# Kernel tuning notes

Hardware: AMD Instinct MI355X
Metric: run time of the kernel (lower is better)

Reference implementation:

```python
import jax, jax.numpy as jnp
import numpy as np

B, T, D_K, N_HEADS, D_FF, VOCAB, N_LAYERS = 4, 1024, 1024, 16, 4096, 65, 6


def setup_inputs() -> dict:
    key = jax.random.key(0)
    ks = jax.random.split(key, 12)
    f = lambda k, sh: jax.random.normal(k, sh, dtype=jnp.float32) * 0.02
    return {
        "batchData": jax.random.randint(ks[0], (B, T), 0, VOCAB),
        "target": jax.random.randint(ks[1], (B, T), 0, VOCAB),
        "pos": jnp.arange(T),
        "Wtok": f(ks[2], (VOCAB, D_K)),
        "Wpos": f(ks[3], (T, D_K)),
        "Wq": f(ks[4], (D_K, D_K)), "bq": jnp.zeros((D_K,), jnp.float32),
        "Wk": f(ks[5], (D_K, D_K)), "bk": jnp.zeros((D_K,), jnp.float32),
        "Wv": f(ks[6], (D_K, D_K)), "bv": jnp.zeros((D_K,), jnp.float32),
        "W1": f(ks[7], (D_K, D_FF)), "b1": jnp.zeros((D_FF,), jnp.float32),
        "W2": f(ks[8], (D_FF, D_K)), "b2": jnp.zeros((D_K,), jnp.float32),
        "ln_w": jnp.ones((D_K,), jnp.float32),
        "Wf": f(ks[9], (D_K, VOCAB)), "bf": jnp.zeros((VOCAB,), jnp.float32),
        "n_layers": N_LAYERS,
        "n_heads": N_HEADS,
    }


def layer_norm(x, w, eps=1e-5):
    m = jnp.mean(x, axis=-1, keepdims=True)
    v = jnp.var(x, axis=-1, keepdims=True)
    return (x - m) / jnp.sqrt(v + eps) * w


def reference(batchData, target, pos, Wtok, Wpos, Wq, bq, Wk, bk, Wv, bv,
              W1, b1, W2, b2, ln_w, Wf, bf, n_layers, n_heads):
    x = Wtok[batchData] + Wpos[pos]  # [B, T, C] (pos embedding broadcasts)
    Bsz, Tlen, C = x.shape
    dh = C // n_heads
    mask = jnp.tril(jnp.ones((Tlen, Tlen), dtype=bool))
    inv_sqrt_dk = 1.0 / jnp.sqrt(jnp.float32(C))  # source divides by sqrt(full d_k)

    def block(x):
        q = (x @ Wq + bq).reshape(Bsz, Tlen, n_heads, dh).transpose(0, 2, 1, 3)
        k = (x @ Wk + bk).reshape(Bsz, Tlen, n_heads, dh).transpose(0, 2, 1, 3)
        v = (x @ Wv + bv).reshape(Bsz, Tlen, n_heads, dh).transpose(0, 2, 1, 3)
        scores = jnp.einsum('bhqd,bhkd->bhqk', q, k) * inv_sqrt_dk
        scores = jnp.where(mask, scores, -jnp.inf)
        attn = jax.nn.softmax(scores, axis=-1)
        h = jnp.einsum('bhqk,bhkd->bhqd', attn, v)
        h = h.transpose(0, 2, 1, 3).reshape(Bsz, Tlen, C)
        h = h + layer_norm(h, ln_w)           # x = x + ln(x) (shared ln)
        ff = jax.nn.relu(h @ W1 + b1) @ W2 + b2
        return ff + layer_norm(ff, ln_w)      # same shared ln again

    # ModuleList repeats the SAME block object, so weights are shared across layers
    for _ in range(n_layers):
        x = block(x)

    logits = x @ Wf + bf                       # [B, T, V]
    probs = jax.nn.softmax(logits, axis=1)     # softmax over T, as in source
    pred = probs.reshape(Bsz * Tlen, -1)
    onehot = jax.nn.one_hot(target.reshape(-1), VOCAB, dtype=jnp.float32)
    # F.cross_entropy with soft (one-hot float) targets
    loss = -jnp.mean(jnp.sum(onehot * jax.nn.log_softmax(pred, axis=-1), axis=-1))
    return loss, probs
```

## Files before the change

### kernel.cpp

```cpp
#include <hip/hip_runtime.h>

typedef __attribute__((ext_vector_type(8))) short bh8;
typedef __attribute__((ext_vector_type(4))) float f4v;

constexpr int VOC = 65;
constexpr int NL  = 6;
constexpr int Mrow = 4096;

__device__ inline float b2f(unsigned short u) {
  union { unsigned int i; float f; } x; x.i = ((unsigned int)u) << 16; return x.f;
}
__device__ inline unsigned short f2b(float f) {
  union { float f; unsigned int i; } x; x.f = f;
  return (unsigned short)((x.i + 0x7FFFu + ((x.i >> 16) & 1u)) >> 16);
}
__device__ inline void gld16(const void* g, void* l) {
  __builtin_amdgcn_global_load_lds(
      (const __attribute__((address_space(1))) unsigned int*)g,
      (__attribute__((address_space(3))) unsigned int*)l, 16, 0, 0);
}
__device__ inline bh8 lds_swz(const unsigned short* base, int row, int colbyte) {
  int off = row * 128 + (colbyte ^ ((row & 7) << 4));
  return *(const bh8*)((const char*)base + off);
}
__device__ inline f4v mfma16(bh8 a, bh8 b, f4v c) {
  return __builtin_amdgcn_mfma_f32_16x16x32_bf16(a, b, c, 0, 0, 0);
}
#define WAITV(n) asm volatile("s_waitcnt vmcnt(" #n ")" ::: "memory")
#define WAITVL(n) asm volatile("s_waitcnt vmcnt(" #n ") lgkmcnt(0)" ::: "memory")

__global__ __launch_bounds__(256) void wt_conv(const float* __restrict__ src,
    unsigned short* __restrict__ dst, int K, int N) {
  __shared__ float t[32][33];
  int k0 = blockIdx.x * 32, n0 = blockIdx.y * 32;
  int tid = threadIdx.x;
#pragma unroll
  for (int i = 0; i < 4; ++i) {
    int idx = tid + i * 256;
    int kr = idx >> 5, nc = idx & 31;
    t[kr][nc] = (n0 + nc < N) ? src[(size_t)(k0 + kr) * N + n0 + nc] : 0.f;
  }
  __syncthreads();
#pragma unroll
  for (int i = 0; i < 4; ++i) {
    int idx = tid + i * 256;
    int nr = idx >> 5, kc = idx & 31;
    dst[(size_t)(n0 + nr) * K + k0 + kc] = f2b(t[kc][nr]);
  }
}

__global__ __launch_bounds__(256) void bias_prep(
    const float* __restrict__ bq, const float* __restrict__ bk,
    const float* __restrict__ bv, const float* __restrict__ bf,
    float* __restrict__ bqkv, float* __restrict__ bfp) {
  int i = blockIdx.x * 256 + threadIdx.x;
  if (i < 1024) bqkv[i] = bq[i];
  else if (i < 2048) bqkv[i] = bk[i - 1024];
  else if (i < 3072) bqkv[i] = bv[i - 2048];
  else if (i < 3200) bfp[i - 3072] = (i - 3072 < VOC) ? bf[i - 3072] : 0.f;
}

__global__ __launch_bounds__(256) void embed_bf(const int* __restrict__ tok,
    const float* __restrict__ Wtok, const float* __restrict__ Wpos,
    unsigned short* __restrict__ Xb) {
  int bt = blockIdx.x, t = bt & 1023, tid = threadIdx.x;
  int id = tok[bt];
  float4 a = ((const float4*)(Wtok + (size_t)id * 1024))[tid];
  float4 p = ((const float4*)(Wpos + (size_t)t * 1024))[tid];
  ushort4 o;
  o.x = f2b(a.x + p.x); o.y = f2b(a.y + p.y);
  o.z = f2b(a.z + p.z); o.w = f2b(a.w + p.w);
  ((ushort4*)(Xb + (size_t)bt * 1024))[tid] = o;
}

template <bool RELU, bool PART, bool VT>
__global__ __launch_bounds__(512) void gemm8(
    const unsigned short* __restrict__ A, const unsigned short* __restrict__ Bt,
    const float* __restrict__ bias, void* __restrict__ Cout,
    unsigned short* __restrict__ Vtout, long N, long Kloop, long lda, long ldb,
    int MT, int NT) {
  __shared__ unsigned short As[3 * 256 * 32];
  __shared__ unsigned short Bs[3 * 128 * 32];
  const int tid = threadIdx.x;
  const int lane = tid & 63, w = tid >> 6;
  const int wr = w >> 1, wc = w & 1;
  const int lr = lane & 15, lh = lane >> 4, lh4 = lh * 4;

  const int nwg = (int)gridDim.x;
  const int wid = ((int)blockIdx.x & 7) * (nwg >> 3) + ((int)blockIdx.x >> 3);
  const int rowT = wid % MT, rest = wid / MT;
  const int colT = rest % NT, ksl = rest / NT;
  const long row0 = (long)rowT * 256, col0 = (long)colT * 128;
  const long kOff = (long)ksl * Kloop;

  f4v acc[4][4];
#pragma unroll
  for (int i = 0; i < 4; ++i)
#pragma unroll
    for (int j = 0; j < 4; ++j) acc[i][j] = f4v{0.f, 0.f, 0.f, 0.f};

  const int rg = tid >> 2, s = tid & 3;
  const int ch = s ^ ((rg ^ (rg >> 2)) & 3);
  const unsigned short* ApA0 = A + (row0 + rg) * lda + kOff + ch * 8;
  const unsigned short* ApA1 = ApA0 + 128 * lda;
  const unsigned short* BpB  = Bt + (col0 + rg) * ldb + kOff + ch * 8;

  auto stage = [&](int t, int buf) {
    const long k0 = (long)t << 5;
    gld16(ApA0 + k0, &As[buf * 8192 + tid * 8]);
    gld16(ApA1 + k0, &As[buf * 8192 + 4096 + tid * 8]);
    gld16(BpB  + k0, &Bs[buf * 4096 + tid * 8]);
  };

  const int nt = (int)(Kloop >> 5);
  stage(0, 0);
  stage(1, 1);

  const int fl = (lr ^ (lr >> 2)) & 3;
  const int slot = lh ^ fl;

  for (int t = 0; t < nt; ++t) {
    if (t + 1 < nt) { WAITVL(3); } else { WAITVL(0); }
    __builtin_amdgcn_s_barrier();
    __builtin_amdgcn_sched_barrier(0);
    const unsigned short* Ab = &As[(t % 3) * 8192];
    const unsigned short* Bb = &Bs[(t % 3) * 4096];
    bh8 a[4], b[4];
#pragma unroll
    for (int mi = 0; mi < 4; ++mi)
      a[mi] = *(const bh8*)&Ab[(wr * 64 + mi * 16 + lr) * 32 + slot * 8];
#pragma unroll
    for (int ni = 0; ni < 4; ++ni)
      b[ni] = *(const bh8*)&Bb[(wc * 64 + ni * 16 + lr) * 32 + slot * 8];
    if (t + 2 < nt) stage(t + 2, (t + 2) % 3);
    __builtin_amdgcn_s_setprio(1);
#pragma unroll
    for (int mi = 0; mi < 4; ++mi)
#pragma unroll
      for (int ni = 0; ni < 4; ++ni)
        acc[mi][ni] = mfma16(a[mi], b[ni], acc[mi][ni]);
    __builtin_amdgcn_s_setprio(0);
  }

  if (PART) {
    unsigned short* P = (unsigned short*)Cout + (size_t)ksl * 4096 * 1024;
#pragma unroll
    for (int mi = 0; mi < 4; ++mi)
#pragma unroll
      for (int ni = 0; ni < 4; ++ni) {
        long col = col0 + wc * 64 + ni * 16 + lr;
#pragma unroll
        for (int r = 0; r < 4; ++r) {
          long row = row0 + wr * 64 + mi * 16 + lh4 + r;
          P[row * N + col] = f2b(acc[mi][ni][r]);
        }
      }
    return;
  }
  if (VT && col0 >= 2048) {
#pragma unroll
    for (int mi = 0; mi < 4; ++mi) {
#pragma unroll
      for (int ni = 0; ni < 4; ++ni) {
        int col = (int)col0 + wc * 64 + ni * 16 + lr;
        float bb = bias[col];
        int cc = col - 2048;
        long row = row0 + wr * 64 + mi * 16 + lh4;
        int bi = (int)(row >> 10), tt = (int)(row & 1023);
        ushort4 o;
        o.x = f2b(acc[mi][ni][0] + bb);
        o.y = f2b(acc[mi][ni][1] + bb);
        o.z = f2b(acc[mi][ni][2] + bb);
        o.w = f2b(acc[mi][ni][3] + bb);
        *(ushort4*)&Vtout[((size_t)(bi * 16 + (cc >> 6)) * 64 + (cc & 63)) *
                              1024 + tt] = o;
      }
    }
    return;
  }
#pragma unroll
  for (int mi = 0; mi < 4; ++mi) {
#pragma unroll
    for (int ni = 0; ni < 4; ++ni) {
      long col = col0 + wc * 64 + ni * 16 + lr;
      float bb = bias[col];
#pragma unroll
      for (int r = 0; r < 4; ++r) {
        long row = row0 + wr * 64 + mi * 16 + lh4 + r;
        float v = acc[mi][ni][r] + bb;
        if (RELU) v = fmaxf(v, 0.f);
        ((unsigned short*)Cout)[row * N + col] = f2b(v);
      }
    }
  }
}

template <int TM, int TN, bool RELU, bool F32OUT>
__global__ __launch_bounds__(256) void gemm4(
    const unsigned short* __restrict__ A, const unsigned short* __restrict__ Bt,
    const float* __restrict__ bias, void* __restrict__ Cout, long N, long K) {
  constexpr int MI = TM / 32, NI = TN / 32;
  constexpr int ABUF = TM * 64, BBUF = TN * 64;
  __shared__ unsigned short As[2 * ABUF];
  __shared__ unsigned short Bs[2 * BBUF];
  const int tid = threadIdx.x;
  const int lane = tid & 63, w = tid >> 6;
  const int wr = w >> 1, wc = w & 1;
  const int lr = lane & 15, lh = lane >> 4, lh4 = lh * 4;
  const long row0 = (long)blockIdx.x * TM, col0 = (long)blockIdx.y * TN;
  f4v acc[MI][NI];
#pragma unroll
  for (int i = 0; i < MI; ++i)
#pragma unroll
    for (int j = 0; j < NI; ++j) acc[i][j] = f4v{0.f, 0.f, 0.f, 0.f};
  const int rg = tid >> 3, s = tid & 7;
  const int ch = s ^ (rg & 7);
  const unsigned short* Ap = A + (row0 + rg) * K + ch * 8;
  const unsigned short* Bp = Bt + (col0 + rg) * K + ch * 8;
  auto stage = [&](int t, int buf) {
    const long k0 = (long)t << 6;
#pragma unroll
    for (int i = 0; i < MI; ++i)
      gld16(Ap + i * 32 * K + k0, &As[buf * ABUF + (i * 256 + tid) * 8]);
#pragma unroll
    for (int i = 0; i < NI; ++i)
      gld16(Bp + i * 32 * K + k0, &Bs[buf * BBUF + (i * 256 + tid) * 8]);
  };
  const int nt = (int)(K >> 6);
  stage(0, 0);
  for (int t = 0; t < nt; ++t) {
    const int cur = t & 1;
    if (t + 1 < nt) {
      stage(t + 1, cur ^ 1);
      WAITV(6);
    } else {
      WAITV(0);
    }
    __builtin_amdgcn_s_barrier();
    const unsigned short* Ab = &As[cur * ABUF];
    const unsigned short* Bb = &Bs[cur * BBUF];
#pragma unroll
    for (int ks = 0; ks < 2; ++ks) {
      bh8 a[MI], b[NI];
      const int slot = ((ks << 2) | lh) ^ (lr & 7);
#pragma unroll
      for (int mi = 0; mi < MI; ++mi) {
        int m = wr * (TM / 2) + mi * 16 + lr;
        a[mi] = *(const bh8*)((const char*)Ab + m * 128 + slot * 16);
      }
#pragma unroll
      for (int ni = 0; ni < NI; ++ni) {
        int n = wc * (TN / 2) + ni * 16 + lr;
        b[ni] = *(const bh8*)((const char*)Bb + n * 128 + slot * 16);
      }
#pragma unroll
      for (int mi = 0; mi < MI; ++mi)
#pragma unroll
        for (int ni = 0; ni < NI; ++ni)
          acc[mi][ni] = mfma16(a[mi], b[ni], acc[mi][ni]);
    }
    __builtin_amdgcn_s_barrier();
  }
#pragma unroll
  for (int mi = 0; mi < MI; ++mi) {
#pragma unroll
    for (int ni = 0; ni < NI; ++ni) {
      long col = col0 + wc * (TN / 2) + ni * 16 + lr;
      float bb = bias[col];
#pragma unroll
      for (int r = 0; r < 4; ++r) {
        long row = row0 + wr * (TM / 2) + mi * 16 + lh4 + r;
        float v = acc[mi][ni][r] + bb;
        if (RELU) v = fmaxf(v, 0.f);
        if (F32OUT) ((float*)Cout)[row * N + col] = v;
        else ((unsigned short*)Cout)[row * N + col] = f2b(v);
      }
    }
  }
}

__global__ __launch_bounds__(256) void attn_mfma(
    const unsigned short* __restrict__ QKV, const unsigned short* __restrict__ Vt,
    unsigned short* __restrict__ Hout) {
  __shared__ unsigned short Ks[2][64 * 64];
  __shared__ unsigned short Vs[2][64 * 64];
  __shared__ unsigned short Ps[4][16 * 64];
  const int tid = threadIdx.x, w = tid >> 6, lane = tid & 63;
  const int qt = (int)gridDim.x - 1 - (int)blockIdx.x;
  const int bh = blockIdx.y;
  const int b = bh >> 4, h = bh & 15;
  const int lr = lane & 15, lh = lane >> 4, lh4 = lh * 4;

  const unsigned short* qp =
      QKV + (size_t)(b * 1024 + qt * 64 + w * 16 + lr) * 3072 + h * 64 + lh * 8;
  bh8 aq0 = *(const bh8*)qp;
  bh8 aq1 = *(const bh8*)(qp + 32);

  f4v o[4];
#pragma unroll
  for (int i = 0; i < 4; ++i) o[i] = f4v{0.f, 0.f, 0.f, 0.f};
  float m = -1e30f, l = 0.f;

  const int r8 = tid >> 3, slot = tid & 7;
  unsigned short* pw = &Ps[w][0];

  auto stage = [&](int kt, int buf) {
    int r = r8, c8 = (slot ^ (r & 7)) * 8;
    gld16(QKV + (size_t)(b * 1024 + kt * 64 + r) * 3072 + 1024 + h * 64 + c8,
          &Ks[buf][tid * 8]);
    gld16(Vt + (size_t)(bh * 64 + r) * 1024 + kt * 64 + c8, &Vs[buf][tid * 8]);
    r = r8 + 32; c8 = (slot ^ (r & 7)) * 8;
    gld16(QKV + (size_t)(b * 1024 + kt * 64 + r) * 3072 + 1024 + h * 64 + c8,
          &Ks[buf][2048 + tid * 8]);
    gld16(Vt + (size_t)(bh * 64 + r) * 1024 + kt * 64 + c8,
          &Vs[buf][2048 + tid * 8]);
  };

  stage(0, 0);

  for (int kt = 0; kt <= qt; ++kt) {
    const int cur = kt & 1;
    if (kt < qt) {
      stage(kt + 1, cur ^ 1);
      WAITV(4);
    } else {
      WAITV(0);
    }
    __builtin_amdgcn_s_barrier();

    f4v s[4];
#pragma unroll
    for (int nt = 0; nt < 4; ++nt) {
      bh8 k0 = lds_swz(Ks[cur], nt * 16 + lr, lh * 16);
      bh8 k1 = lds_swz(Ks[cur], nt * 16 + lr, lh * 16 + 64);
      f4v z = f4v{0.f, 0.f, 0.f, 0.f};
      z = mfma16(k0, aq0, z);
      z = mfma16(k1, aq1, z);
      s[nt] = z;
    }
    const bool diag = (kt == qt);
    const int qloc = w * 16 + lr;
#pragma unroll
    for (int nt = 0; nt < 4; ++nt)
#pragma unroll
      for (int r = 0; r < 4; ++r) {
        float v = s[nt][r] * 0.03125f;
        if (diag && (nt * 16 + lh4 + r) > qloc) v = -1e30f;
        s[nt][r] = v;
      }
    float tm = s[0][0];
#pragma unroll
    for (int nt = 0; nt < 4; ++nt)
#pragma unroll
      for (int r = 0; r < 4; ++r) tm = fmaxf(tm, s[nt][r]);
    tm = fmaxf(tm, __shfl_xor(tm, 16));
    tm = fmaxf(tm, __shfl_xor(tm, 32));
    float mn = fmaxf(m, tm);
    float corr = __expf(m - mn);
    m = mn;
    float sum = 0.f;
#pragma unroll
    for (int nt = 0; nt < 4; ++nt)
#pragma unroll
      for (int r = 0; r < 4; ++r) {
        float e = __expf(s[nt][r] - mn);
        s[nt][r] = e;
        sum += e;
      }
    sum += __shfl_xor(sum, 16);
    sum += __shfl_xor(sum, 32);
    l = l * corr + sum;
#pragma unroll
    for (int nt = 0; nt < 4; ++nt) {
      unsigned int u0, u1;
      asm("v_cvt_pk_bf16_f32 %0, %1, %2" : "=v"(u0) : "v"(s[nt][0]), "v"(s[nt][1]));
      asm("v_cvt_pk_bf16_f32 %0, %1, %2" : "=v"(u1) : "v"(s[nt][2]), "v"(s[nt][3]));
      uint2 pk{u0, u1};
      *(uint2*)((char*)pw + lr * 128 + ((nt * 32 + lh * 8) ^ ((lr & 7) << 4))) = pk;
    }
    float c0 = __shfl(corr, lh4 + 0), c1 = __shfl(corr, lh4 + 1);
    float c2 = __shfl(corr, lh4 + 2), c3 = __shfl(corr, lh4 + 3);
#pragma unroll
    for (int nt = 0; nt < 4; ++nt) {
      o[nt][0] *= c0; o[nt][1] *= c1; o[nt][2] *= c2; o[nt][3] *= c3;
    }
    bh8 pa0 = lds_swz(pw, lr, lh * 16);
    bh8 pa1 = lds_swz(pw, lr, lh * 16 + 64);
#pragma unroll
    for (int nt = 0; nt < 4; ++nt) {
      bh8 v0 = lds_swz(Vs[cur], nt * 16 + lr, lh * 16);
      bh8 v1 = lds_swz(Vs[cur], nt * 16 + lr, lh * 16 + 64);
      o[nt] = mfma16(pa0, v0, o[nt]);
      o[nt] = mfma16(pa1, v1, o[nt]);
    }
    __builtin_amdgcn_s_barrier();
  }
  float linv = 1.f / l;
  float l0 = __shfl(linv, lh4 + 0), l1 = __shfl(linv, lh4 + 1);
  float l2 = __shfl(linv, lh4 + 2), l3 = __shfl(linv, lh4 + 3);
  const size_t rowb = (size_t)(b * 1024 + qt * 64 + w * 16);
#pragma unroll
  for (int nt = 0; nt < 4; ++nt) {
    int col = h * 64 + nt * 16 + lr;
    Hout[(rowb + lh4 + 0) * 1024 + col] = f2b(o[nt][0] * l0);
    Hout[(rowb + lh4 + 1) * 1024 + col] = f2b(o[nt][1] * l1);
    Hout[(rowb + lh4 + 2) * 1024 + col] = f2b(o[nt][2] * l2);
    Hout[(rowb + lh4 + 3) * 1024 + col] = f2b(o[nt][3] * l3);
  }
}

__global__ __launch_bounds__(256) void ln_res_bf(
    const unsigned short* __restrict__ Xi, const float* __restrict__ wln,
    unsigned short* __restrict__ Y) {
  int row = blockIdx.x, tid = threadIdx.x;
  ushort4 u = ((const ushort4*)(Xi + (size_t)row * 1024))[tid];
  float x0 = b2f(u.x), x1 = b2f(u.y), x2 = b2f(u.z), x3 = b2f(u.w);
  float s = x0 + x1 + x2 + x3;
  float ss = x0 * x0 + x1 * x1 + x2 * x2 + x3 * x3;
#pragma unroll
  for (int off = 32; off; off >>= 1) {
    s += __shfl_xor(s, off);
    ss += __shfl_xor(ss, off);
  }
  __shared__ float sw[4], ssw[4];
  int wv = tid >> 6, ln = tid & 63;
  if (ln == 0) { sw[wv] = s; ssw[wv] = ss; }
  __syncthreads();
  s = sw[0] + sw[1] + sw[2] + sw[3];
  ss = ssw[0] + ssw[1] + ssw[2] + ssw[3];
  float mean = s * (1.f / 1024.f);
  float var = ss * (1.f / 1024.f) - mean * mean;
  float rstd = rsqrtf(var + 1e-5f);
  float4 wv4 = ((const float4*)wln)[tid];
  ushort4 out;
  out.x = f2b(x0 + (x0 - mean) * rstd * wv4.x);
  out.y = f2b(x1 + (x1 - mean) * rstd * wv4.y);
  out.z = f2b(x2 + (x2 - mean) * rstd * wv4.z);
  out.w = f2b(x3 + (x3 - mean) * rstd * wv4.w);
  ((ushort4*)(Y + (size_t)row * 1024))[tid] = out;
}

__global__ __launch_bounds__(256) void ln2_fuse(
    const unsigned short* __restrict__ P, const float* __restrict__ b2,
    const float* __restrict__ wln, unsigned short* __restrict__ Y) {
  int row = blockIdx.x, tid = threadIdx.x;
  const size_t plane = (size_t)4096 * 1024;
  float x0 = 0.f, x1 = 0.f, x2 = 0.f, x3 = 0.f;
#pragma unroll
  for (int pl = 0; pl < 4; ++pl) {
    ushort4 u = *(const ushort4*)&P[pl * plane + (size_t)row * 1024 + tid * 4];
    x0 += b2f(u.x); x1 += b2f(u.y); x2 += b2f(u.z); x3 += b2f(u.w);
  }
  float4 bb = ((const float4*)b2)[tid];
  x0 += bb.x; x1 += bb.y; x2 += bb.z; x3 += bb.w;
  float s = x0 + x1 + x2 + x3;
  float ss = x0 * x0 + x1 * x1 + x2 * x2 + x3 * x3;
#pragma unroll
  for (int off = 32; off; off >>= 1) {
    s += __shfl_xor(s, off);
    ss += __shfl_xor(ss, off);
  }
  __shared__ float sw[4], ssw[4];
  int wv = tid >> 6, ln = tid & 63;
  if (ln == 0) { sw[wv] = s; ssw[wv] = ss; }
  __syncthreads();
  s = sw[0] + sw[1] + sw[2] + sw[3];
  ss = ssw[0] + ssw[1] + ssw[2] + ssw[3];
  float mean = s * (1.f / 1024.f);
  float var = ss * (1.f / 1024.f) - mean * mean;
  float rstd = rsqrtf(var + 1e-5f);
  float4 wv4 = ((const float4*)wln)[tid];
  ushort4 out;
  out.x = f2b(x0 + (x0 - mean) * rstd * wv4.x);
  out.y = f2b(x1 + (x1 - mean) * rstd * wv4.y);
  out.z = f2b(x2 + (x2 - mean) * rstd * wv4.z);
  out.w = f2b(x3 + (x3 - mean) * rstd * wv4.w);
  ((ushort4*)(Y + (size_t)row * 1024))[tid] = out;
}

__global__ __launch_bounds__(256) void softmaxT_kernel(
    const float* __restrict__ logits, float* __restrict__ probs) {
  int b = blockIdx.x / VOC;
  int v = blockIdx.x - b * VOC;
  const float* src = logits + (size_t)b * 1024 * 128 + v;
  float vals[4];
  float m = -1e30f;
#pragma unroll
  for (int i = 0; i < 4; ++i) {
    int t = threadIdx.x + 256 * i;
    vals[i] = src[(size_t)t * 128];
    m = fmaxf(m, vals[i]);
  }
#pragma unroll
  for (int off = 32; off; off >>= 1) m = fmaxf(m, __shfl_xor(m, off));
  __shared__ float sm[4], ssum[4];
  int wv = threadIdx.x >> 6, ln = threadIdx.x & 63;
  if (ln == 0) sm[wv] = m;
  __syncthreads();
  m = fmaxf(fmaxf(sm[0], sm[1]), fmaxf(sm[2], sm[3]));
  float s = 0.f;
#pragma unroll
  for (int i = 0; i < 4; ++i) { vals[i] = __expf(vals[i] - m); s += vals[i]; }
#pragma unroll
  for (int off = 32; off; off >>= 1) s += __shfl_xor(s, off);
  if (ln == 0) ssum[wv] = s;
  __syncthreads();
  s = ssum[0] + ssum[1] + ssum[2] + ssum[3];
  float inv = 1.f / s;
  float* dst = probs + (size_t)b * 1024 * VOC + v;
#pragma unroll
  for (int i = 0; i < 4; ++i) {
    int t = threadIdx.x + 256 * i;
    dst[(size_t)t * VOC] = vals[i] * inv;
  }
}

__global__ __launch_bounds__(256) void loss_rows_kernel(
    const float* __restrict__ probs, const int* __restrict__ tgt,
    float* __restrict__ partial) {
  int wv = threadIdx.x >> 6, lane = threadIdx.x & 63;
  int row = blockIdx.x * 4 + wv;
  const float* p = probs + (size_t)row * VOC;
  float x0 = p[lane];
  float x1 = (lane == 0) ? p[64] : -1e30f;
  float m = fmaxf(x0, x1);
#pragma unroll
  for (int off = 32; off; off >>= 1) m = fmaxf(m, __shfl_xor(m, off));
  float s = __expf(x0 - m) + ((lane == 0) ? __expf(x1 - m) : 0.f);
#pragma unroll
  for (int off = 32; off; off >>= 1) s += __shfl_xor(s, off);
  if (lane == 0) {
    int tg = tgt[row];
    partial[row] = (p[tg] - m) - logf(s);
  }
}

__global__ __launch_bounds__(256) void loss_final_kernel(
    const float* __restrict__ partial, float* __restrict__ out) {
  float s = 0.f;
  for (int i = threadIdx.x; i < Mrow; i += 256) s += partial[i];
#pragma unroll
  for (int off = 32; off; off >>= 1) s += __shfl_xor(s, off);
  __shared__ float sw[4];
  int wv = threadIdx.x >> 6, ln = threadIdx.x & 63;
  if (ln == 0) sw[wv] = s;
  __syncthreads();
  if (threadIdx.x == 0) out[0] = -(sw[0] + sw[1] + sw[2] + sw[3]) / (float)Mrow;
}

extern "C" void kernel_launch(void* const* d_in, const int* in_sizes, int n_in,
                              void* d_out, int out_size, void* d_ws,
                              size_t ws_size, hipStream_t stream) {
  (void)in_sizes; (void)n_in; (void)out_size; (void)ws_size;
  const int*   tok    = (const int*)d_in[0];
  const int*   target = (const int*)d_in[1];
  const float* Wtok   = (const float*)d_in[3];
  const float* Wpos   = (const float*)d_in[4];
  const float* Wq = (const float*)d_in[5];  const float* bq = (const float*)d_in[6];
  const float* Wk = (const float*)d_in[7];  const float* bk = (const float*)d_in[8];
  const float* Wv = (const float*)d_in[9];  const float* bv = (const float*)d_in[10];
  const float* W1 = (const float*)d_in[11]; const float* b1 = (const float*)d_in[12];
  const float* W2 = (const float*)d_in[13]; const float* b2 = (const float*)d_in[14];
  const float* lnw = (const float*)d_in[15];
  const float* Wf = (const float*)d_in[16]; const float* bf = (const float*)d_in[17];
  float* out = (float*)d_out;

  char* p = (char*)d_ws;
  unsigned short* Xb    = (unsigned short*)p; p += (size_t)Mrow * 1024 * 2;
  unsigned short* QKVb  = (unsigned short*)p; p += (size_t)Mrow * 3072 * 2;
  unsigned short* Vt    = (unsigned short*)p; p += (size_t)64 * 64 * 1024 * 2;
  unsigned short* Hb    = (unsigned short*)p; p += (size_t)Mrow * 1024 * 2;
  unsigned short* F2b   = (unsigned short*)p; p += (size_t)Mrow * 1024 * 2;
  unsigned short* FF1b  = (unsigned short*)p; p += (size_t)Mrow * 4096 * 2;
  unsigned short* WqkvT = (unsigned short*)p; p += (size_t)3072 * 1024 * 2;
  unsigned short* W1T   = (unsigned short*)p; p += (size_t)4096 * 1024 * 2;
  unsigned short* W2T   = (unsigned short*)p; p += (size_t)1024 * 4096 * 2;
  unsigned short* WfT   = (unsigned short*)p; p += (size_t)128 * 1024 * 2;
  float* bqkv = (float*)p; p += 3072 * 4;
  float* bfp  = (float*)p; p += 128 * 4;
  float* LOG  = (float*)p; p += (size_t)Mrow * 128 * 4;
  float* PART = (float*)p; p += Mrow * 4;
  unsigned short* Pff2 = QKVb;

  wt_conv<<<dim3(32, 32), 256, 0, stream>>>(Wq, WqkvT,                1024, 1024);
  wt_conv<<<dim3(32, 32), 256, 0, stream>>>(Wk, WqkvT + 1024 * 1024,  1024, 1024);
  wt_conv<<<dim3(32, 32), 256, 0, stream>>>(Wv, WqkvT + 2048 * 1024,  1024, 1024);
  wt_conv<<<dim3(32, 128), 256, 0, stream>>>(W1, W1T, 1024, 4096);
  wt_conv<<<dim3(128, 32), 256, 0, stream>>>(W2, W2T, 4096, 1024);
  wt_conv<<<dim3(32, 4), 256, 0, stream>>>(Wf, WfT, 1024, VOC);
  bias_prep<<<13, 256, 0, stream>>>(bq, bk, bv, bf, bqkv, bfp);

  embed_bf<<<Mrow, 256, 0, stream>>>(tok, Wtok, Wpos, Xb);

  for (int l = 0; l < NL; ++l) {
    gemm8<false, false, true><<<384, 512, 0, stream>>>(
        Xb, WqkvT, bqkv, QKVb, Vt, 3072, 1024, 1024, 1024, 16, 24);
    attn_mfma<<<dim3(16, 64), 256, 0, stream>>>(QKVb, Vt, Hb);
    ln_res_bf<<<Mrow, 256, 0, stream>>>(Hb, lnw, F2b);
    gemm8<true, false, false><<<512, 512, 0, stream>>>(
        F2b, W1T, b1, FF1b, nullptr, 4096, 1024, 1024, 1024, 16, 32);
    gemm8<false, true, false><<<512, 512, 0, stream>>>(
        FF1b, W2T, nullptr, Pff2, nullptr, 1024, 1024, 4096, 4096, 16, 8);
    ln2_fuse<<<Mrow, 256, 0, stream>>>(Pff2, b2, lnw, Xb);
  }

  gemm4<64, 128, false, true><<<dim3(64, 1), 256, 0, stream>>>(
      Xb, WfT, bfp, LOG, 128, 1024);
  softmaxT_kernel<<<4 * VOC, 256, 0, stream>>>(LOG, out + 1);
  loss_rows_kernel<<<Mrow / 4, 256, 0, stream>>>(out + 1, target, PART);
  loss_final_kernel<<<1, 256, 0, stream>>>(PART, out);
}
```

Measured before the change: 1.048 ms.

## Add BM-templated gemm8 with 128-row QKV tiles, fold Q scale, lazy softmax rescale

Templates gemm8 on row-tile size so the QKV projection runs with 128-row tiles and 256 threads over twice as many workgroups, for better fill across CUs. The 1/32 attention scale is folded into the Q projection epilogue, which removes a multiply per score. Attention now applies the causal mask only on diagonal tiles. It rescales the running max, sum and output accumulator only when some row's max grows by more than 8 (a lazy-rescale trick), which drops exp and multiply work on most tiles. The cost is extra branching, plus some exposure to bf16 rounding from rounding Q after the scale and from softmax values that are not rescaled.

```diff
diff --git a/kernel.cpp b/kernel.cpp
--- a/kernel.cpp
+++ b/kernel.cpp
@@ -27,7 +27,16 @@
   return __builtin_amdgcn_mfma_f32_16x16x32_bf16(a, b, c, 0, 0, 0);
 }
 #define WAITV(n) asm volatile("s_waitcnt vmcnt(" #n ")" ::: "memory")
-#define WAITVL(n) asm volatile("s_waitcnt vmcnt(" #n ") lgkmcnt(0)" ::: "memory")
+template <int N> __device__ inline void waitvl() {
+  if constexpr (N == 0)
+    asm volatile("s_waitcnt vmcnt(0) lgkmcnt(0)" ::: "memory");
+  else if constexpr (N == 3)
+    asm volatile("s_waitcnt vmcnt(3) lgkmcnt(0)" ::: "memory");
+  else if constexpr (N == 4)
+    asm volatile("s_waitcnt vmcnt(4) lgkmcnt(0)" ::: "memory");
+  else
+    asm volatile("s_waitcnt vmcnt(6) lgkmcnt(0)" ::: "memory");
+}
 
 __global__ __launch_bounds__(256) void wt_conv(const float* __restrict__ src,
     unsigned short* __restrict__ dst, int K, int N) {
@@ -73,13 +82,17 @@
   ((ushort4*)(Xb + (size_t)bt * 1024))[tid] = o;
 }
 
-template <bool RELU, bool PART, bool VT>
-__global__ __launch_bounds__(512) void gemm8(
+template <int BM, bool RELU, bool PART, bool VT>
+__global__ __launch_bounds__((BM == 256 ? 512 : 256)) void gemm8(
     const unsigned short* __restrict__ A, const unsigned short* __restrict__ Bt,
     const float* __restrict__ bias, void* __restrict__ Cout,
     unsigned short* __restrict__ Vtout, long N, long Kloop, long lda, long ldb,
     int MT, int NT) {
-  __shared__ unsigned short As[3 * 256 * 32];
+  constexpr int T = (BM == 256 ? 512 : 256);
+  constexpr int RPL = T / 4;
+  constexpr int LA = BM / RPL, LB = 128 / RPL;
+  constexpr int LNUM = LA + LB;
+  __shared__ unsigned short As[3 * BM * 32];
   __shared__ unsigned short Bs[3 * 128 * 32];
   const int tid = threadIdx.x;
   const int lane = tid & 63, w = tid >> 6;
@@ -90,7 +103,7 @@
   const int wid = ((int)blockIdx.x & 7) * (nwg >> 3) + ((int)blockIdx.x >> 3);
   const int rowT = wid % MT, rest = wid / MT;
   const int colT = rest % NT, ksl = rest / NT;
-  const long row0 = (long)rowT * 256, col0 = (long)colT * 128;
+  const long row0 = (long)rowT * BM, col0 = (long)colT * 128;
   const long kOff = (long)ksl * Kloop;
 
   f4v acc[4][4];
@@ -101,15 +114,17 @@
 
   const int rg = tid >> 2, s = tid & 3;
   const int ch = s ^ ((rg ^ (rg >> 2)) & 3);
-  const unsigned short* ApA0 = A + (row0 + rg) * lda + kOff + ch * 8;
-  const unsigned short* ApA1 = ApA0 + 128 * lda;
-  const unsigned short* BpB  = Bt + (col0 + rg) * ldb + kOff + ch * 8;
+  const unsigned short* Ap = A + (row0 + rg) * lda + kOff + ch * 8;
+  const unsigned short* Bp = Bt + (col0 + rg) * ldb + kOff + ch * 8;
 
   auto stage = [&](int t, int buf) {
     const long k0 = (long)t << 5;
-    gld16(ApA0 + k0, &As[buf * 8192 + tid * 8]);
-    gld16(ApA1 + k0, &As[buf * 8192 + 4096 + tid * 8]);
-    gld16(BpB  + k0, &Bs[buf * 4096 + tid * 8]);
+#pragma unroll
+    for (int i = 0; i < LA; ++i)
+      gld16(Ap + (long)i * RPL * lda + k0, &As[buf * BM * 32 + (i * T + tid) * 8]);
+#pragma unroll
+    for (int i = 0; i < LB; ++i)
+      gld16(Bp + (long)i * RPL * ldb + k0, &Bs[buf * 4096 + (i * T + tid) * 8]);
   };
 
   const int nt = (int)(Kloop >> 5);
@@ -120,10 +135,10 @@
   const int slot = lh ^ fl;
 
   for (int t = 0; t < nt; ++t) {
-    if (t + 1 < nt) { WAITVL(3); } else { WAITVL(0); }
+    if (t + 1 < nt) { waitvl<LNUM>(); } else { waitvl<0>(); }
     __builtin_amdgcn_s_barrier();
     __builtin_amdgcn_sched_barrier(0);
-    const unsigned short* Ab = &As[(t % 3) * 8192];
+    const unsigned short* Ab = &As[(t % 3) * BM * 32];
     const unsigned short* Bb = &Bs[(t % 3) * 4096];
     bh8 a[4], b[4];
 #pragma unroll
@@ -178,6 +193,7 @@
     }
     return;
   }
+  const float qsc = (VT && col0 < 1024) ? 0.03125f : 1.0f;
 #pragma unroll
   for (int mi = 0; mi < 4; ++mi) {
 #pragma unroll
@@ -188,6 +204,7 @@
       for (int r = 0; r < 4; ++r) {
         long row = row0 + wr * 64 + mi * 16 + lh4 + r;
         float v = acc[mi][ni][r] + bb;
+        if (VT) v *= qsc;
         if (RELU) v = fmaxf(v, 0.f);
         ((unsigned short*)Cout)[row * N + col] = f2b(v);
       }
@@ -339,37 +356,48 @@
       s[nt] = z;
     }
     const bool diag = (kt == qt);
-    const int qloc = w * 16 + lr;
-#pragma unroll
-    for (int nt = 0; nt < 4; ++nt)
-#pragma unroll
-      for (int r = 0; r < 4; ++r) {
-        float v = s[nt][r] * 0.03125f;
-        if (diag && (nt * 16 + lh4 + r) > qloc) v = -1e30f;
-        s[nt][r] = v;
-      }
-    float tm = s[0][0];
-#pragma unroll
-    for (int nt = 0; nt < 4; ++nt)
-#pragma unroll
-      for (int r = 0; r < 4; ++r) tm = fmaxf(tm, s[nt][r]);
+    if (diag) {
+      const int qloc = w * 16 + lr;
+#pragma unroll
+      for (int nt = 0; nt < 4; ++nt)
+#pragma unroll
+        for (int r = 0; r < 4; ++r)
+          if ((nt * 16 + lh4 + r) > qloc) s[nt][r] = -1e30f;
+    }
+    float tm = fmaxf(fmaxf(fmaxf(s[0][0], s[0][1]), fmaxf(s[0][2], s[0][3])),
+                     fmaxf(fmaxf(s[1][0], s[1][1]), fmaxf(s[1][2], s[1][3])));
+    float tm2 = fmaxf(fmaxf(fmaxf(s[2][0], s[2][1]), fmaxf(s[2][2], s[2][3])),
+                      fmaxf(fmaxf(s[3][0], s[3][1]), fmaxf(s[3][2], s[3][3])));
+    tm = fmaxf(tm, tm2);
     tm = fmaxf(tm, __shfl_xor(tm, 16));
     tm = fmaxf(tm, __shfl_xor(tm, 32));
-    float mn = fmaxf(m, tm);
-    float corr = __expf(m - mn);
-    m = mn;
+
+    const bool resc = __any(tm > m + 8.f);
+    const float mu = resc ? fmaxf(m, tm) : m;
     float sum = 0.f;
 #pragma unroll
     for (int nt = 0; nt < 4; ++nt)
 #pragma unroll
       for (int r = 0; r < 4; ++r) {
-        float e = __expf(s[nt][r] - mn);
+        float e = __expf(s[nt][r] - mu);
         s[nt][r] = e;
         sum += e;
       }
     sum += __shfl_xor(sum, 16);
     sum += __shfl_xor(sum, 32);
-    l = l * corr + sum;
+    if (resc) {
+      float corr = __expf(m - mu);
+      m = mu;
+      l = l * corr + sum;
+      float c0 = __shfl(corr, lh4 + 0), c1 = __shfl(corr, lh4 + 1);
+      float c2 = __shfl(corr, lh4 + 2), c3 = __shfl(corr, lh4 + 3);
+#pragma unroll
+      for (int nt = 0; nt < 4; ++nt) {
+        o[nt][0] *= c0; o[nt][1] *= c1; o[nt][2] *= c2; o[nt][3] *= c3;
+      }
+    } else {
+      l += sum;
+    }
 #pragma unroll
     for (int nt = 0; nt < 4; ++nt) {
       unsigned int u0, u1;
@@ -377,12 +405,6 @@
       asm("v_cvt_pk_bf16_f32 %0, %1, %2" : "=v"(u1) : "v"(s[nt][2]), "v"(s[nt][3]));
       uint2 pk{u0, u1};
       *(uint2*)((char*)pw + lr * 128 + ((nt * 32 + lh * 8) ^ ((lr & 7) << 4))) = pk;
-    }
-    float c0 = __shfl(corr, lh4 + 0), c1 = __shfl(corr, lh4 + 1);
-    float c2 = __shfl(corr, lh4 + 2), c3 = __shfl(corr, lh4 + 3);
-#pragma unroll
-    for (int nt = 0; nt < 4; ++nt) {
-      o[nt][0] *= c0; o[nt][1] *= c1; o[nt][2] *= c2; o[nt][3] *= c3;
     }
     bh8 pa0 = lds_swz(pw, lr, lh * 16);
     bh8 pa1 = lds_swz(pw, lr, lh * 16 + 64);
@@ -593,13 +615,13 @@
   embed_bf<<<Mrow, 256, 0, stream>>>(tok, Wtok, Wpos, Xb);
 
   for (int l = 0; l < NL; ++l) {
-    gemm8<false, false, true><<<384, 512, 0, stream>>>(
-        Xb, WqkvT, bqkv, QKVb, Vt, 3072, 1024, 1024, 1024, 16, 24);
+    gemm8<128, false, false, true><<<768, 256, 0, stream>>>(
+        Xb, WqkvT, bqkv, QKVb, Vt, 3072, 1024, 1024, 1024, 32, 24);
     attn_mfma<<<dim3(16, 64), 256, 0, stream>>>(QKVb, Vt, Hb);
     ln_res_bf<<<Mrow, 256, 0, stream>>>(Hb, lnw, F2b);
-    gemm8<true, false, false><<<512, 512, 0, stream>>>(
+    gemm8<256, true, false, false><<<512, 512, 0, stream>>>(
         F2b, W1T, b1, FF1b, nullptr, 4096, 1024, 1024, 1024, 16, 32);
-    gemm8<false, true, false><<<512, 512, 0, stream>>>(
+    gemm8<256, false, true, false><<<512, 512, 0, stream>>>(
         FF1b, W2T, nullptr, Pff2, nullptr, 1024, 1024, 4096, 4096, 16, 8);
     ln2_fuse<<<Mrow, 256, 0, stream>>>(Pff2, b2, lnw, Xb);
   }
```

Result: slower. 1.079 ms (+3.0%).
